# Performance work log

Hardware: AMD Instinct MI355X
Metric: run time of the kernel (lower is better)

Reference implementation:

```python
import jax, jax.numpy as jnp
import numpy as np

TAU_MIN, TAU_MAX = 1.5, 4.0
NUM_EXPERTS, TOP_K = 8, 2
V_TH = 1.0
BN_EPS = 1e-5
SG_ALPHA = 4.0  # spikingjelly Sigmoid surrogate default

@jax.custom_vjp
def spike(v):
    # Heaviside spike with sigmoid surrogate gradient
    return (v >= 0.0).astype(v.dtype)

def _spike_fwd(v):
    return spike(v), v

def _spike_bwd(v, g):
    s = jax.nn.sigmoid(SG_ALPHA * v)
    return (g * SG_ALPHA * s * (1.0 - s),)

spike.defvjp(_spike_fwd, _spike_bwd)

def lif(x, tau):
    # MultiStepLIFNode, v_reset=0 (hard reset), detach_reset=True. x: (T, ...)
    def step(v, xt):
        v = v + (xt - v) / tau          # charge
        s = spike(v - V_TH)             # fire
        v = v * (1.0 - jax.lax.stop_gradient(s))  # detached hard reset
        return v, s
    return jax.lax.scan(step, jnp.zeros_like(x[0]), x)[1]

def conv1x1(x, W, b):
    # x: (T,B,Cin,H,W), W: (Cout,Cin) -> (T,B,Cout,H,W)
    return jnp.einsum('tbchw,oc->tbohw', x, W) + b[None, None, :, None, None]

def bn_eval(x, scale, bias):
    # eval-mode BatchNorm2d with running_mean=0, running_var=1
    inv = scale / jnp.sqrt(1.0 + BN_EPS)
    return x * inv[None, None, :, None, None] + bias[None, None, :, None, None]

def expert_fwd(x, tau, W1, b1, s1, bb1, W2, b2, s2, bb2):
    # MS_MLP_Expert: LIF -> conv1x1 -> BN -> (+res) -> LIF -> conv1x1 -> BN -> (+res)
    identity = x
    h = lif(x, tau)
    h = bn_eval(conv1x1(h, W1, b1), s1, bb1)
    h = identity + h            # res: in_features == hidden_features
    identity = h
    o = lif(h, tau)
    o = bn_eval(conv1x1(o, W2, b2), s2, bb2)
    return o + identity

def moe_forward(x, router_W, router_b, router_bn_scale, router_bn_bias,
                W1, b1, bn1_scale, bn1_bias, W2, b2, bn2_scale, bn2_bias):
    T, B, C, H, W = x.shape
    taus = jnp.linspace(TAU_MIN, TAU_MAX, NUM_EXPERTS).astype(x.dtype)
    # --- SpikeRouter ---
    r = lif(x, 2.0)
    r = bn_eval(conv1x1(r, router_W, router_b), router_bn_scale, router_bn_bias)  # (T,B,E,H,W)
    logits_tb = r.mean(axis=(-2, -1))          # (T,B,E)
    # batch-level temporal routing: aggregate logits over T
    logits = logits_tb.mean(axis=0)            # (B,E)
    probs = jax.nn.softmax(logits, axis=-1)
    topw, topi = jax.lax.top_k(probs, TOP_K)   # (B,k)
    topw = topw / topw.sum(axis=-1, keepdims=True)
    dense_w = jnp.zeros((B, NUM_EXPERTS), dtype=x.dtype).at[
        jnp.arange(B)[:, None], topi].set(topw)  # (B,E)
    # --- experts: each processes the full temporal sequence ---
    ys = jax.vmap(expert_fwd, in_axes=(None, 0, 0, 0, 0, 0, 0, 0, 0, 0))(
        x, taus, W1, b1, bn1_scale, bn1_bias, W2, b2, bn2_scale, bn2_bias)  # (E,T,B,C,H,W)
    out = jnp.einsum('etbchw,be->tbchw', ys, dense_w)
    return out

def setup_inputs() -> dict:
    key = jax.random.key(0)
    ks = jax.random.split(key, 6)
    T, B, C, H, Wd = 4, 16, 384, 16, 16
    E = NUM_EXPERTS
    wscale = 1.0 / np.sqrt(C)
    return {
        'x': jax.random.normal(ks[0], (T, B, C, H, Wd), jnp.float32),
        'router_W': jax.random.normal(ks[1], (E, C), jnp.float32) * wscale,
        'router_b': jnp.zeros((E,), jnp.float32),
        'router_bn_scale': jnp.ones((E,), jnp.float32),
        'router_bn_bias': jnp.zeros((E,), jnp.float32),
        'W1': jax.random.normal(ks[2], (E, C, C), jnp.float32) * wscale,
        'b1': jnp.zeros((E, C), jnp.float32),
        'bn1_scale': jnp.ones((E, C), jnp.float32),
        'bn1_bias': jnp.zeros((E, C), jnp.float32),
        'W2': jax.random.normal(ks[3], (E, C, C), jnp.float32) * wscale,
        'b2': jnp.zeros((E, C), jnp.float32),
        'bn2_scale': jnp.ones((E, C), jnp.float32),
        'bn2_bias': jnp.zeros((E, C), jnp.float32),
    }

def reference(x, router_W, router_b, router_bn_scale, router_bn_bias,
              W1, b1, bn1_scale, bn1_bias, W2, b2, bn2_scale, bn2_bias):
    return moe_forward(x, router_W, router_b, router_bn_scale, router_bn_bias,
                       W1, b1, bn1_scale, bn1_bias, W2, b2, bn2_scale, bn2_bias)
```

## Files before the change

### kernel.cpp

```cpp
#include <hip/hip_runtime.h>
#include <math.h>

#define T_  4
#define B_  16
#define C_  384
#define HW_ 256
#define E_  8

typedef __attribute__((ext_vector_type(8))) __bf16 bf16x8;
typedef __attribute__((ext_vector_type(4))) float f32x4;

union FragU { uint4 u; bf16x8 v; };

__device__ __forceinline__ float tau_of(int e) {
    if (e == 7) return 4.0f;
    const float delta = 2.5f / 7.0f;
    return __fadd_rn(1.5f, __fmul_rn((float)e, delta));
}

__device__ __forceinline__ FragU expand_mask(unsigned m) {
    FragU f;
    f.u.x = ((m & 1u)   ? 0x3F80u : 0u) | ((m & 2u)   ? 0x3F800000u : 0u);
    f.u.y = ((m & 4u)   ? 0x3F80u : 0u) | ((m & 8u)   ? 0x3F800000u : 0u);
    f.u.z = ((m & 16u)  ? 0x3F80u : 0u) | ((m & 32u)  ? 0x3F800000u : 0u);
    f.u.w = ((m & 64u)  ? 0x3F80u : 0u) | ((m & 128u) ? 0x3F800000u : 0u);
    return f;
}

__global__ __launch_bounds__(256) void k_prep(const float* __restrict__ x,
        const float* __restrict__ W1, const float* __restrict__ W2,
        unsigned short* __restrict__ Whif, unsigned short* __restrict__ Wlof,
        float* __restrict__ m) {
    if (blockIdx.x < 1152) {
        int tid = blockIdx.x * 256 + threadIdx.x;
        int l = tid & 63;
        int f = tid >> 6;
        int osub = f % 24;
        int ksub = (f / 24) % 12;
        int cv = (f / 288) & 1;
        int e = f / 576;
        const float* Wsrc = (cv == 0 ? W1 : W2) + (size_t)e * C_ * C_;
        int o = osub * 16 + (l & 15);
        int c0 = ksub * 32 + (l >> 4) * 8;
        const float* src = Wsrc + (size_t)o * C_ + c0;
        unsigned hw[8], lw[8];
#pragma unroll
        for (int j = 0; j < 8; ++j) {
            float w = src[j];
            unsigned u = __float_as_uint(w);
            unsigned hi = (u + 0x7FFFu + ((u >> 16) & 1u)) >> 16;
            float hf = __uint_as_float(hi << 16);
            float res = __fsub_rn(w, hf);
            unsigned ru = __float_as_uint(res);
            unsigned lo = (ru + 0x7FFFu + ((ru >> 16) & 1u)) >> 16;
            hw[j] = hi & 0xFFFFu;
            lw[j] = lo & 0xFFFFu;
        }
        size_t dst = (size_t)f * 512 + (size_t)l * 8;
        uint4 hv = make_uint4(hw[0] | (hw[1] << 16), hw[2] | (hw[3] << 16),
                              hw[4] | (hw[5] << 16), hw[6] | (hw[7] << 16));
        uint4 lv = make_uint4(lw[0] | (lw[1] << 16), lw[2] | (lw[3] << 16),
                              lw[4] | (lw[5] << 16), lw[6] | (lw[7] << 16));
        *reinterpret_cast<uint4*>(Whif + dst) = hv;
        *reinterpret_cast<uint4*>(Wlof + dst) = lv;
    } else {
        int bc = blockIdx.x - 1152;
        int b = bc / C_, c = bc % C_;
        int p = threadIdx.x;
        int wv = threadIdx.x >> 6;
        __shared__ int cnt[T_][4];
        float v = 0.0f;
#pragma unroll
        for (int t = 0; t < T_; ++t) {
            float xv = x[((t * B_ + b) * C_ + c) * HW_ + p];
            v = __fadd_rn(v, __fdiv_rn(__fsub_rn(xv, v), 2.0f));
            bool s = (__fsub_rn(v, 1.0f) >= 0.0f);
            if (s) v = 0.0f;
            unsigned long long mask = __ballot(s);
            if ((threadIdx.x & 63) == 0) cnt[t][wv] = (int)__popcll(mask);
        }
        __syncthreads();
        if (threadIdx.x < T_) {
            int t = threadIdx.x;
            int tot = cnt[t][0] + cnt[t][1] + cnt[t][2] + cnt[t][3];
            m[(t * B_ + b) * C_ + c] = (float)tot * 0.00390625f;
        }
    }
}

__device__ __forceinline__ void conv_mfma(const unsigned short* __restrict__ Whif,
                                          const unsigned short* __restrict__ Wlof,
                                          unsigned base,
                                          const unsigned char* __restrict__ sm,
                                          f32x4 (&acc)[3][4],
                                          int wave, int lane, int q, int pl) {
    const unsigned lane8 = (unsigned)lane * 8u;
    const unsigned wbase = base + (unsigned)(wave * 3) * 512u + lane8;
    FragU c0f, c1f, c2f, n0f, n1f, n2f;
    c0f.u = *reinterpret_cast<const uint4*>(Wlof + wbase);
    c1f.u = *reinterpret_cast<const uint4*>(Wlof + wbase + 512u);
    c2f.u = *reinterpret_cast<const uint4*>(Wlof + wbase + 1024u);
#pragma unroll 1
    for (int ksub = 0; ksub < 12; ++ksub) {
        unsigned fo = wbase + (unsigned)ksub * 24u * 512u;
        FragU bf[T_];
#pragma unroll
        for (int t = 0; t < T_; ++t) {
            unsigned mbyte = sm[(t * 16 + pl) * 48 + ksub * 4 + q];
            bf[t] = expand_mask(mbyte);
        }
        n0f.u = *reinterpret_cast<const uint4*>(Whif + fo);
        n1f.u = *reinterpret_cast<const uint4*>(Whif + fo + 512u);
        n2f.u = *reinterpret_cast<const uint4*>(Whif + fo + 1024u);
#pragma unroll
        for (int t = 0; t < T_; ++t) {
            acc[0][t] = __builtin_amdgcn_mfma_f32_16x16x32_bf16(c0f.v, bf[t].v, acc[0][t], 0, 0, 0);
            acc[1][t] = __builtin_amdgcn_mfma_f32_16x16x32_bf16(c1f.v, bf[t].v, acc[1][t], 0, 0, 0);
            acc[2][t] = __builtin_amdgcn_mfma_f32_16x16x32_bf16(c2f.v, bf[t].v, acc[2][t], 0, 0, 0);
        }
        if (ksub < 11) {
            unsigned fn = fo + 24u * 512u;
            c0f.u = *reinterpret_cast<const uint4*>(Wlof + fn);
            c1f.u = *reinterpret_cast<const uint4*>(Wlof + fn + 512u);
            c2f.u = *reinterpret_cast<const uint4*>(Wlof + fn + 1024u);
        }
#pragma unroll
        for (int t = 0; t < T_; ++t) {
            acc[0][t] = __builtin_amdgcn_mfma_f32_16x16x32_bf16(n0f.v, bf[t].v, acc[0][t], 0, 0, 0);
            acc[1][t] = __builtin_amdgcn_mfma_f32_16x16x32_bf16(n1f.v, bf[t].v, acc[1][t], 0, 0, 0);
            acc[2][t] = __builtin_amdgcn_mfma_f32_16x16x32_bf16(n2f.v, bf[t].v, acc[2][t], 0, 0, 0);
        }
    }
}

__global__ __launch_bounds__(512, 2) void k_expert(
        const float* __restrict__ x, const float* __restrict__ m,
        const float* __restrict__ rW, const float* __restrict__ rb,
        const float* __restrict__ rbs, const float* __restrict__ rbb,
        const unsigned short* __restrict__ Whif, const unsigned short* __restrict__ Wlof,
        const float* __restrict__ b1, const float* __restrict__ s1sc, const float* __restrict__ s1bi,
        const float* __restrict__ b2, const float* __restrict__ s2sc, const float* __restrict__ s2bi,
        float* __restrict__ out) {
    int blk = blockIdx.x;
    int b = (blk & 7) | (((blk >> 3) & 1) << 3);
    int ptile = blk >> 4;

    __shared__ unsigned char s1m[2][T_ * 16 * 48];
    __shared__ unsigned char s2m[2][T_ * 16 * 48];
    __shared__ float bns[2 * 6 * C_];
    __shared__ float lg[E_];
    __shared__ float wsl[2];
    __shared__ int esl[2];

    int tid = threadIdx.x;
    int wave = tid >> 6;
    int lane = tid & 63;
    int q = lane >> 4;
    int pl = lane & 15;
    int p = ptile * 16 + pl;
    float denom = sqrtf(__fadd_rn(1.0f, 1e-5f));

    if (tid < 64) {
        int combo = tid & 31, half = tid >> 5;
        int e = combo >> 2, t = combo & 3;
        float dot = 0.0f;
        int c0 = half * 192;
        for (int c = 0; c < 192; ++c)
            dot = fmaf(rW[e * C_ + c0 + c], m[(t * B_ + b) * C_ + c0 + c], dot);
        dot += __shfl_down(dot, 32);
        float Ar = __fdiv_rn(rbs[e], denom);
        float lt = __fadd_rn(__fmul_rn(__fadd_rn(dot, rb[e]), Ar), rbb[e]);
        lt = __fadd_rn(lt, __shfl_xor(lt, 1));
        lt = __fadd_rn(lt, __shfl_xor(lt, 2));
        if (half == 0 && t == 0) lg[e] = __fmul_rn(lt, 0.25f);
    }
    __syncthreads();
    if (tid == 0) {
        float pr[E_];
        float mx = lg[0];
        for (int i = 1; i < E_; ++i) mx = fmaxf(mx, lg[i]);
        float s = 0.0f;
        for (int i = 0; i < E_; ++i) { pr[i] = expf(__fsub_rn(lg[i], mx)); s = __fadd_rn(s, pr[i]); }
        for (int i = 0; i < E_; ++i) pr[i] = __fdiv_rn(pr[i], s);
        int i0 = 0;
        for (int i = 1; i < E_; ++i) if (pr[i] > pr[i0]) i0 = i;
        int i1 = (i0 == 0) ? 1 : 0;
        for (int i = 0; i < E_; ++i) if (i != i0 && pr[i] > pr[i1]) i1 = i;
        float s2 = __fadd_rn(pr[i0], pr[i1]);
        wsl[0] = __fdiv_rn(pr[i0], s2);
        wsl[1] = __fdiv_rn(pr[i1], s2);
        esl[0] = i0;
        esl[1] = i1;
    }
    __syncthreads();

    int e0 = esl[0], e1 = esl[1];
    float tau0 = tau_of(e0), tau1 = tau_of(e1);

    if (tid < C_) {
#pragma unroll
        for (int r_ = 0; r_ < 2; ++r_) {
            int er = (r_ == 0) ? e0 : e1;
            bns[(r_ * 6 + 0) * C_ + tid] = __fdiv_rn(s1sc[er * C_ + tid], denom);
            bns[(r_ * 6 + 1) * C_ + tid] = b1[er * C_ + tid];
            bns[(r_ * 6 + 2) * C_ + tid] = s1bi[er * C_ + tid];
            bns[(r_ * 6 + 3) * C_ + tid] = __fdiv_rn(s2sc[er * C_ + tid], denom);
            bns[(r_ * 6 + 4) * C_ + tid] = b2[er * C_ + tid];
            bns[(r_ * 6 + 5) * C_ + tid] = s2bi[er * C_ + tid];
        }
    }

#pragma unroll 1
    for (int task = tid; task < 48 * 16; task += 512) {
        int cb = task >> 4;
        int tpl = task & 15;
        int tp = ptile * 16 + tpl;
        float va[8], vb[8];
#pragma unroll
        for (int j = 0; j < 8; ++j) { va[j] = 0.0f; vb[j] = 0.0f; }
#pragma unroll
        for (int t = 0; t < T_; ++t) {
            int gbase = ((t * B_ + b) * C_ + cb * 8) * HW_ + tp;
            unsigned mb0 = 0, mb1 = 0;
#pragma unroll
            for (int j = 0; j < 8; ++j) {
                float xv = x[gbase + j * HW_];
                va[j] = __fadd_rn(va[j], __fdiv_rn(__fsub_rn(xv, va[j]), tau0));
                if (__fsub_rn(va[j], 1.0f) >= 0.0f) { mb0 |= (1u << j); va[j] = 0.0f; }
                vb[j] = __fadd_rn(vb[j], __fdiv_rn(__fsub_rn(xv, vb[j]), tau1));
                if (__fsub_rn(vb[j], 1.0f) >= 0.0f) { mb1 |= (1u << j); vb[j] = 0.0f; }
            }
            s1m[0][(t * 16 + tpl) * 48 + cb] = (unsigned char)mb0;
            s1m[1][(t * 16 + tpl) * 48 + cb] = (unsigned char)mb1;
        }
    }
    __syncthreads();

    float part[3][4][4];
#pragma unroll
    for (int os = 0; os < 3; ++os)
#pragma unroll
        for (int t = 0; t < T_; ++t)
#pragma unroll
            for (int r = 0; r < 4; ++r) part[os][t][r] = 0.0f;

#pragma unroll 1
    for (int r_ = 0; r_ < 2; ++r_) {
        int er = (r_ == 0) ? e0 : e1;
        float wr = wsl[r_];
        float taur = (r_ == 0) ? tau0 : tau1;
        unsigned base1 = (unsigned)(er * 2) * 12u * 24u * 512u;

        f32x4 acc[3][4];
#pragma unroll
        for (int os = 0; os < 3; ++os)
#pragma unroll
            for (int t = 0; t < T_; ++t) acc[os][t] = (f32x4)0.0f;

        conv_mfma(Whif, Wlof, base1, &s1m[r_][0], acc, wave, lane, q, pl);

#pragma unroll
        for (int os = 0; os < 3; ++os) {
            float v2s[4] = {0.f, 0.f, 0.f, 0.f};
#pragma unroll
            for (int t = 0; t < T_; ++t) {
                unsigned nb = 0;
#pragma unroll
                for (int r = 0; r < 4; ++r) {
                    int o = wave * 48 + os * 16 + q * 4 + r;
                    int gi = ((t * B_ + b) * C_ + o) * HW_ + p;
                    float y = acc[os][t][r];
                    float h = __fadd_rn(x[gi],
                        __fadd_rn(__fmul_rn(__fadd_rn(y, bns[(r_ * 6 + 1) * C_ + o]),
                                            bns[(r_ * 6 + 0) * C_ + o]),
                                  bns[(r_ * 6 + 2) * C_ + o]));
                    part[os][t][r] = fmaf(wr, h, part[os][t][r]);
                    v2s[r] = __fadd_rn(v2s[r], __fdiv_rn(__fsub_rn(h, v2s[r]), taur));
                    if (__fsub_rn(v2s[r], 1.0f) >= 0.0f) { nb |= (1u << r); v2s[r] = 0.f; }
                }
                unsigned nb_hi = (unsigned)__shfl_down((int)nb, 16);
                if ((q & 1) == 0) {
                    int cbyte = wave * 6 + os * 2 + (q >> 1);
                    s2m[r_][(t * 16 + pl) * 48 + cbyte] = (unsigned char)(nb | (nb_hi << 4));
                }
            }
        }
    }
    __syncthreads();

#pragma unroll 1
    for (int r_ = 0; r_ < 2; ++r_) {
        int er = (r_ == 0) ? e0 : e1;
        float wr = wsl[r_];
        unsigned base2 = (unsigned)(er * 2 + 1) * 12u * 24u * 512u;

        f32x4 acc[3][4];
#pragma unroll
        for (int os = 0; os < 3; ++os)
#pragma unroll
            for (int t = 0; t < T_; ++t) acc[os][t] = (f32x4)0.0f;

        conv_mfma(Whif, Wlof, base2, &s2m[r_][0], acc, wave, lane, q, pl);

#pragma unroll
        for (int os = 0; os < 3; ++os)
#pragma unroll
            for (int t = 0; t < T_; ++t)
#pragma unroll
                for (int r = 0; r < 4; ++r) {
                    int o = wave * 48 + os * 16 + q * 4 + r;
                    float y = acc[os][t][r];
                    float val = __fadd_rn(__fmul_rn(__fadd_rn(y, bns[(r_ * 6 + 4) * C_ + o]),
                                                    bns[(r_ * 6 + 3) * C_ + o]),
                                          bns[(r_ * 6 + 5) * C_ + o]);
                    part[os][t][r] = fmaf(wr, val, part[os][t][r]);
                }
    }

#pragma unroll
    for (int os = 0; os < 3; ++os)
#pragma unroll
        for (int t = 0; t < T_; ++t)
#pragma unroll
            for (int r = 0; r < 4; ++r) {
                int o = wave * 48 + os * 16 + q * 4 + r;
                int gi = ((t * B_ + b) * C_ + o) * HW_ + p;
                out[gi] = part[os][t][r];
            }
}

extern "C" void kernel_launch(void* const* d_in, const int* in_sizes, int n_in,
                              void* d_out, int out_size, void* d_ws, size_t ws_size,
                              hipStream_t stream) {
    const float* x    = (const float*)d_in[0];
    const float* rW   = (const float*)d_in[1];
    const float* rb   = (const float*)d_in[2];
    const float* rbs  = (const float*)d_in[3];
    const float* rbb  = (const float*)d_in[4];
    const float* W1   = (const float*)d_in[5];
    const float* b1   = (const float*)d_in[6];
    const float* s1sc = (const float*)d_in[7];
    const float* s1bi = (const float*)d_in[8];
    const float* W2   = (const float*)d_in[9];
    const float* b2   = (const float*)d_in[10];
    const float* s2sc = (const float*)d_in[11];
    const float* s2bi = (const float*)d_in[12];
    float* out = (float*)d_out;

    unsigned short* Whif = (unsigned short*)d_ws;
    unsigned short* Wlof = Whif + 2359296;
    float* m = (float*)((char*)d_ws + 9437184);

    hipLaunchKernelGGL(k_prep, dim3(1152 + B_ * C_), dim3(256), 0, stream,
                       x, W1, W2, Whif, Wlof, m);
    hipLaunchKernelGGL(k_expert, dim3(256), dim3(512), 0, stream,
                       x, m, rW, rb, rbs, rbb, Whif, Wlof,
                       b1, s1sc, s1bi, b2, s2sc, s2bi, out);
}
```

Before: 161.4 us.

## Run both routed experts concurrently in 1024-thread blocks with pre-expanded LDS fragments

Each block doubles to 1024 threads, and two 512-thread ranks each handle one of the two selected experts in parallel instead of looping over them. Spike masks are now stored in LDS as pre-expanded bf16 MFMA fragments, so the conv inner loop does one vector load instead of byte loads plus mask expansion. The layer-1 residual is folded into the layer-2 accumulator by pre-scaling with the reciprocal BN scale, and the two experts' outputs are combined through LDS. This uses much more LDS (about 96KB per block) and tighter launch bounds, which may pressure registers or cause spills. The reciprocal-scale fold also slightly changes rounding.

```diff
diff --git a/kernel.cpp b/kernel.cpp
--- a/kernel.cpp
+++ b/kernel.cpp
@@ -88,27 +88,26 @@
     }
 }
 
-__device__ __forceinline__ void conv_mfma(const unsigned short* __restrict__ Whif,
-                                          const unsigned short* __restrict__ Wlof,
-                                          unsigned base,
-                                          const unsigned char* __restrict__ sm,
-                                          f32x4 (&acc)[3][4],
-                                          int wave, int lane, int q, int pl) {
+__device__ __forceinline__ void conv_mfma2(const unsigned short* __restrict__ Whif,
+                                           const unsigned short* __restrict__ Wlof,
+                                           unsigned base,
+                                           const unsigned char* __restrict__ sf,
+                                           f32x4 (&acc)[3][4],
+                                           int wv, int lane) {
     const unsigned lane8 = (unsigned)lane * 8u;
-    const unsigned wbase = base + (unsigned)(wave * 3) * 512u + lane8;
-    FragU c0f, c1f, c2f, n0f, n1f, n2f;
+    const unsigned wbase = base + (unsigned)(wv * 3) * 512u + lane8;
+    const unsigned char* fp = sf + lane * 16;
+    FragU c0f, c1f, c2f, n0f, n1f, n2f, bf[T_];
     c0f.u = *reinterpret_cast<const uint4*>(Wlof + wbase);
     c1f.u = *reinterpret_cast<const uint4*>(Wlof + wbase + 512u);
     c2f.u = *reinterpret_cast<const uint4*>(Wlof + wbase + 1024u);
 #pragma unroll 1
     for (int ksub = 0; ksub < 12; ++ksub) {
         unsigned fo = wbase + (unsigned)ksub * 24u * 512u;
-        FragU bf[T_];
-#pragma unroll
-        for (int t = 0; t < T_; ++t) {
-            unsigned mbyte = sm[(t * 16 + pl) * 48 + ksub * 4 + q];
-            bf[t] = expand_mask(mbyte);
-        }
+        const unsigned char* fk = fp + ksub * 4096;
+#pragma unroll
+        for (int t = 0; t < T_; ++t)
+            bf[t].u = *reinterpret_cast<const uint4*>(fk + t * 1024);
         n0f.u = *reinterpret_cast<const uint4*>(Whif + fo);
         n1f.u = *reinterpret_cast<const uint4*>(Whif + fo + 512u);
         n2f.u = *reinterpret_cast<const uint4*>(Whif + fo + 1024u);
@@ -133,7 +132,7 @@
     }
 }
 
-__global__ __launch_bounds__(512, 2) void k_expert(
+__global__ __launch_bounds__(1024, 4) void k_expert(
         const float* __restrict__ x, const float* __restrict__ m,
         const float* __restrict__ rW, const float* __restrict__ rb,
         const float* __restrict__ rbs, const float* __restrict__ rbb,
@@ -145,15 +144,17 @@
     int b = (blk & 7) | (((blk >> 3) & 1) << 3);
     int ptile = blk >> 4;
 
-    __shared__ unsigned char s1m[2][T_ * 16 * 48];
-    __shared__ unsigned char s2m[2][T_ * 16 * 48];
-    __shared__ float bns[2 * 6 * C_];
+    __shared__ __align__(16) unsigned char sfrag[2][49152];
+    __shared__ float bns[2 * 7 * C_];
     __shared__ float lg[E_];
     __shared__ float wsl[2];
     __shared__ int esl[2];
 
     int tid = threadIdx.x;
     int wave = tid >> 6;
+    int rank = wave >> 3;
+    int wv = wave & 7;
+    int rtid = tid & 511;
     int lane = tid & 63;
     int q = lane >> 4;
     int pl = lane & 15;
@@ -194,139 +195,143 @@
     }
     __syncthreads();
 
-    int e0 = esl[0], e1 = esl[1];
-    float tau0 = tau_of(e0), tau1 = tau_of(e1);
-
-    if (tid < C_) {
-#pragma unroll
-        for (int r_ = 0; r_ < 2; ++r_) {
-            int er = (r_ == 0) ? e0 : e1;
-            bns[(r_ * 6 + 0) * C_ + tid] = __fdiv_rn(s1sc[er * C_ + tid], denom);
-            bns[(r_ * 6 + 1) * C_ + tid] = b1[er * C_ + tid];
-            bns[(r_ * 6 + 2) * C_ + tid] = s1bi[er * C_ + tid];
-            bns[(r_ * 6 + 3) * C_ + tid] = __fdiv_rn(s2sc[er * C_ + tid], denom);
-            bns[(r_ * 6 + 4) * C_ + tid] = b2[er * C_ + tid];
-            bns[(r_ * 6 + 5) * C_ + tid] = s2bi[er * C_ + tid];
-        }
-    }
-
+    int er = esl[rank];
+    float wr = wsl[rank];
+    float taur = tau_of(er);
+
+    if (rtid < C_) {
+        float* bp = bns + rank * 7 * C_;
+        float a1 = __fdiv_rn(s1sc[er * C_ + rtid], denom);
+        float a2 = __fdiv_rn(s2sc[er * C_ + rtid], denom);
+        bp[0 * C_ + rtid] = a1;
+        bp[1 * C_ + rtid] = b1[er * C_ + rtid];
+        bp[2 * C_ + rtid] = s1bi[er * C_ + rtid];
+        bp[3 * C_ + rtid] = a2;
+        bp[4 * C_ + rtid] = b2[er * C_ + rtid];
+        bp[5 * C_ + rtid] = s2bi[er * C_ + rtid];
+        bp[6 * C_ + rtid] = __fdiv_rn(1.0f, a2);
+    }
+
+    unsigned char* sf = &sfrag[rank][0];
 #pragma unroll 1
-    for (int task = tid; task < 48 * 16; task += 512) {
+    for (int task = rtid; task < 48 * 16; task += 512) {
         int cb = task >> 4;
         int tpl = task & 15;
         int tp = ptile * 16 + tpl;
-        float va[8], vb[8];
-#pragma unroll
-        for (int j = 0; j < 8; ++j) { va[j] = 0.0f; vb[j] = 0.0f; }
+        unsigned char* dst = sf + (cb >> 2) * 4096 + (((cb & 3) * 16 + tpl) * 16);
+        float v[8];
+#pragma unroll
+        for (int j = 0; j < 8; ++j) v[j] = 0.0f;
 #pragma unroll
         for (int t = 0; t < T_; ++t) {
             int gbase = ((t * B_ + b) * C_ + cb * 8) * HW_ + tp;
-            unsigned mb0 = 0, mb1 = 0;
+            unsigned d0 = 0, d1 = 0, d2 = 0, d3 = 0;
 #pragma unroll
             for (int j = 0; j < 8; ++j) {
                 float xv = x[gbase + j * HW_];
-                va[j] = __fadd_rn(va[j], __fdiv_rn(__fsub_rn(xv, va[j]), tau0));
-                if (__fsub_rn(va[j], 1.0f) >= 0.0f) { mb0 |= (1u << j); va[j] = 0.0f; }
-                vb[j] = __fadd_rn(vb[j], __fdiv_rn(__fsub_rn(xv, vb[j]), tau1));
-                if (__fsub_rn(vb[j], 1.0f) >= 0.0f) { mb1 |= (1u << j); vb[j] = 0.0f; }
+                v[j] = __fadd_rn(v[j], __fdiv_rn(__fsub_rn(xv, v[j]), taur));
+                bool s = (__fsub_rn(v[j], 1.0f) >= 0.0f);
+                if (s) v[j] = 0.0f;
+                unsigned bitv = s ? ((j & 1) ? 0x3F800000u : 0x3F80u) : 0u;
+                if (j < 2) d0 |= bitv;
+                else if (j < 4) d1 |= bitv;
+                else if (j < 6) d2 |= bitv;
+                else d3 |= bitv;
             }
-            s1m[0][(t * 16 + tpl) * 48 + cb] = (unsigned char)mb0;
-            s1m[1][(t * 16 + tpl) * 48 + cb] = (unsigned char)mb1;
-        }
-    }
-    __syncthreads();
-
-    float part[3][4][4];
+            *reinterpret_cast<uint4*>(dst + t * 1024) = make_uint4(d0, d1, d2, d3);
+        }
+    }
+    __syncthreads();
+
+    f32x4 acc[3][T_];
 #pragma unroll
     for (int os = 0; os < 3; ++os)
 #pragma unroll
-        for (int t = 0; t < T_; ++t)
-#pragma unroll
-            for (int r = 0; r < 4; ++r) part[os][t][r] = 0.0f;
-
-#pragma unroll 1
-    for (int r_ = 0; r_ < 2; ++r_) {
-        int er = (r_ == 0) ? e0 : e1;
-        float wr = wsl[r_];
-        float taur = (r_ == 0) ? tau0 : tau1;
-        unsigned base1 = (unsigned)(er * 2) * 12u * 24u * 512u;
-
-        f32x4 acc[3][4];
+        for (int t = 0; t < T_; ++t) acc[os][t] = (f32x4)0.0f;
+    unsigned base1 = (unsigned)(er * 2) * 12u * 24u * 512u;
+    conv_mfma2(Whif, Wlof, base1, sf, acc, wv, lane);
+
+    const float* bp = bns + rank * 7 * C_;
+    unsigned pk[3];
+#pragma unroll
+    for (int os = 0; os < 3; ++os) {
+        float v2s[4] = {0.f, 0.f, 0.f, 0.f};
+        unsigned pkos = 0;
+#pragma unroll
+        for (int t = 0; t < T_; ++t) {
+            unsigned nb = 0;
+#pragma unroll
+            for (int r = 0; r < 4; ++r) {
+                int o = wv * 48 + os * 16 + q * 4 + r;
+                int gi = ((t * B_ + b) * C_ + o) * HW_ + p;
+                float y = acc[os][t][r];
+                float h = __fadd_rn(x[gi],
+                    __fadd_rn(__fmul_rn(__fadd_rn(y, bp[1 * C_ + o]), bp[0 * C_ + o]),
+                              bp[2 * C_ + o]));
+                v2s[r] = __fadd_rn(v2s[r], __fdiv_rn(__fsub_rn(h, v2s[r]), taur));
+                if (__fsub_rn(v2s[r], 1.0f) >= 0.0f) { nb |= (1u << r); v2s[r] = 0.f; }
+                acc[os][t][r] = __fmul_rn(h, bp[6 * C_ + o]);
+            }
+            unsigned nb_hi = (unsigned)__shfl_down((int)nb, 16);
+            pkos |= ((nb | (nb_hi << 4)) & 0xFFu) << (8 * t);
+        }
+        pk[os] = pkos;
+    }
+    __syncthreads();
+
+    if ((q & 1) == 0) {
+#pragma unroll
+        for (int os = 0; os < 3; ++os) {
+            int g = wv * 6 + os * 2 + (q >> 1);
+            unsigned char* dst = sf + (g >> 2) * 4096 + (((g & 3) * 16 + pl) * 16);
+#pragma unroll
+            for (int t = 0; t < T_; ++t) {
+                FragU f = expand_mask((pk[os] >> (8 * t)) & 0xFFu);
+                *reinterpret_cast<uint4*>(dst + t * 1024) = f.u;
+            }
+        }
+    }
+    __syncthreads();
+
+    unsigned base2 = (unsigned)(er * 2 + 1) * 12u * 24u * 512u;
+    conv_mfma2(Whif, Wlof, base2, sf, acc, wv, lane);
+
+    __syncthreads();
+
+    float* pcomb = reinterpret_cast<float*>(&sfrag[0][0]);
+    if (rank == 0) {
 #pragma unroll
         for (int os = 0; os < 3; ++os)
 #pragma unroll
-            for (int t = 0; t < T_; ++t) acc[os][t] = (f32x4)0.0f;
-
-        conv_mfma(Whif, Wlof, base1, &s1m[r_][0], acc, wave, lane, q, pl);
-
-#pragma unroll
-        for (int os = 0; os < 3; ++os) {
-            float v2s[4] = {0.f, 0.f, 0.f, 0.f};
-#pragma unroll
-            for (int t = 0; t < T_; ++t) {
-                unsigned nb = 0;
+            for (int t = 0; t < T_; ++t)
 #pragma unroll
                 for (int r = 0; r < 4; ++r) {
-                    int o = wave * 48 + os * 16 + q * 4 + r;
+                    int o = wv * 48 + os * 16 + q * 4 + r;
+                    float y = acc[os][t][r];
+                    float val = __fadd_rn(__fmul_rn(__fadd_rn(y, bp[4 * C_ + o]),
+                                                    bp[3 * C_ + o]),
+                                          bp[5 * C_ + o]);
+                    pcomb[(t * C_ + o) * 16 + pl] = __fmul_rn(wr, val);
+                }
+    }
+    __syncthreads();
+    if (rank == 1) {
+#pragma unroll
+        for (int os = 0; os < 3; ++os)
+#pragma unroll
+            for (int t = 0; t < T_; ++t)
+#pragma unroll
+                for (int r = 0; r < 4; ++r) {
+                    int o = wv * 48 + os * 16 + q * 4 + r;
                     int gi = ((t * B_ + b) * C_ + o) * HW_ + p;
                     float y = acc[os][t][r];
-                    float h = __fadd_rn(x[gi],
-                        __fadd_rn(__fmul_rn(__fadd_rn(y, bns[(r_ * 6 + 1) * C_ + o]),
-                                            bns[(r_ * 6 + 0) * C_ + o]),
-                                  bns[(r_ * 6 + 2) * C_ + o]));
-                    part[os][t][r] = fmaf(wr, h, part[os][t][r]);
-                    v2s[r] = __fadd_rn(v2s[r], __fdiv_rn(__fsub_rn(h, v2s[r]), taur));
-                    if (__fsub_rn(v2s[r], 1.0f) >= 0.0f) { nb |= (1u << r); v2s[r] = 0.f; }
+                    float val = __fadd_rn(__fmul_rn(__fadd_rn(y, bp[4 * C_ + o]),
+                                                    bp[3 * C_ + o]),
+                                          bp[5 * C_ + o]);
+                    out[gi] = __fadd_rn(pcomb[(t * C_ + o) * 16 + pl],
+                                        __fmul_rn(wr, val));
                 }
-                unsigned nb_hi = (unsigned)__shfl_down((int)nb, 16);
-                if ((q & 1) == 0) {
-                    int cbyte = wave * 6 + os * 2 + (q >> 1);
-                    s2m[r_][(t * 16 + pl) * 48 + cbyte] = (unsigned char)(nb | (nb_hi << 4));
-                }
-            }
-        }
-    }
-    __syncthreads();
-
-#pragma unroll 1
-    for (int r_ = 0; r_ < 2; ++r_) {
-        int er = (r_ == 0) ? e0 : e1;
-        float wr = wsl[r_];
-        unsigned base2 = (unsigned)(er * 2 + 1) * 12u * 24u * 512u;
-
-        f32x4 acc[3][4];
-#pragma unroll
-        for (int os = 0; os < 3; ++os)
-#pragma unroll
-            for (int t = 0; t < T_; ++t) acc[os][t] = (f32x4)0.0f;
-
-        conv_mfma(Whif, Wlof, base2, &s2m[r_][0], acc, wave, lane, q, pl);
-
-#pragma unroll
-        for (int os = 0; os < 3; ++os)
-#pragma unroll
-            for (int t = 0; t < T_; ++t)
-#pragma unroll
-                for (int r = 0; r < 4; ++r) {
-                    int o = wave * 48 + os * 16 + q * 4 + r;
-                    float y = acc[os][t][r];
-                    float val = __fadd_rn(__fmul_rn(__fadd_rn(y, bns[(r_ * 6 + 4) * C_ + o]),
-                                                    bns[(r_ * 6 + 3) * C_ + o]),
-                                          bns[(r_ * 6 + 5) * C_ + o]);
-                    part[os][t][r] = fmaf(wr, val, part[os][t][r]);
-                }
-    }
-
-#pragma unroll
-    for (int os = 0; os < 3; ++os)
-#pragma unroll
-        for (int t = 0; t < T_; ++t)
-#pragma unroll
-            for (int r = 0; r < 4; ++r) {
-                int o = wave * 48 + os * 16 + q * 4 + r;
-                int gi = ((t * B_ + b) * C_ + o) * HW_ + p;
-                out[gi] = part[os][t][r];
-            }
+    }
 }
 
 extern "C" void kernel_launch(void* const* d_in, const int* in_sizes, int n_in,
@@ -353,7 +358,7 @@
 
     hipLaunchKernelGGL(k_prep, dim3(1152 + B_ * C_), dim3(256), 0, stream,
                        x, W1, W2, Whif, Wlof, m);
-    hipLaunchKernelGGL(k_expert, dim3(256), dim3(512), 0, stream,
+    hipLaunchKernelGGL(k_expert, dim3(256), dim3(1024), 0, stream,
                        x, m, rW, rb, rbs, rbb, Whif, Wlof,
                        b1, s1sc, s1bi, b2, s2sc, s2bi, out);
 }
```

New measurement: 186.5 us. 1.16x slower.
